# Performance work log

Measured on AMD Instinct MI355X. Metric: run time of the kernel, lower is better.

Reference implementation:

```python
import jax, jax.numpy as jnp
import numpy as np

DT = 0.1  # fixed RK4 step size from the constructor

def setup_inputs() -> dict:
    key = jax.random.key(0)
    k1, k2, k3 = jax.random.split(key, 3)
    B, U, H = 65536, 128, 512
    x0 = jax.random.normal(k1, (B, U), dtype=jnp.float32)
    # small init so 20 unrolled RK4 steps stay numerically tame
    W1 = jax.random.normal(k2, (U, H), dtype=jnp.float32) * (0.5 / np.sqrt(U))
    b1 = jnp.zeros((H,), dtype=jnp.float32)
    W2 = jax.random.normal(k3, (H, U), dtype=jnp.float32) * (0.5 / np.sqrt(H))
    b2 = jnp.zeros((U,), dtype=jnp.float32)
    return {"x0": x0, "W1": W1, "b1": b1, "W2": W2, "b2": b2}

def _mlp(x, W1, b1, W2, b2):
    # vector field: Dense(512, relu) -> Dense(128); time-independent
    return jnp.maximum(x @ W1 + b1, 0.0) @ W2 + b2

def _rk4_integrate(x, n_steps, W1, b1, W2, b2):
    def step(x, _):
        k1 = _mlp(x, W1, b1, W2, b2)
        k2 = _mlp(x + 0.5 * DT * k1, W1, b1, W2, b2)
        k3 = _mlp(x + 0.5 * DT * k2, W1, b1, W2, b2)
        k4 = _mlp(x + DT * k3, W1, b1, W2, b2)
        return x + (DT / 6.0) * (k1 + 2.0 * k2 + 2.0 * k3 + k4), None
    x, _ = jax.lax.scan(step, x, None, length=n_steps)
    return x

def reference(x0, W1, b1, W2, b2):
    # phase 1: integrate t in [0, t1/2 = 1.0] -> 10 RK4 steps at dt=0.1
    x = _rk4_integrate(x0, 10, W1, b1, W2, b2)
    # phase 2: n=5 macro-steps of length (1.0 - 0.0)/5 = 0.2 -> 2 RK4 steps each
    def macro(x, _):
        x = _rk4_integrate(x, 2, W1, b1, W2, b2)
        return x, None
    x, _ = jax.lax.scan(macro, x, None, length=5)
    return x
```

## Files before the change

kernel.cpp:

```cpp
#include <hip/hip_runtime.h>
#include <stdint.h>


typedef _Float16 half8 __attribute__((ext_vector_type(8)));
typedef float f32x4 __attribute__((ext_vector_type(4)));
typedef __attribute__((address_space(3))) char lchar;
typedef __attribute__((address_space(1))) char gchar;

#define KSTR 136

static __device__ __forceinline__ void gload_lds16(const void* g, void* l) {
  __builtin_amdgcn_global_load_lds((const gchar*)g, (lchar*)l, 16, 0, 0);
}

static __device__ __forceinline__ unsigned short f2h(float x) {
  union { _Float16 h; unsigned short u; } cv;
  cv.h = (_Float16)x;
  return cv.u;
}
static __device__ __forceinline__ float h2f(unsigned short u) {
  union { unsigned short u; _Float16 h; } cv;
  cv.u = u;
  return (float)cv.h;
}

__global__ void pack_w(const float* __restrict__ W1, const float* __restrict__ W2,
                       unsigned short* __restrict__ wp) {
  int id = blockIdx.x * 256 + threadIdx.x;
  int lane = id & 63, fid = (id >> 6) & 255;
  int g = lane >> 4, lm = lane & 15;
  int c = fid >> 4, f = fid & 15;
  if (f < 8) {
    int nt = f >> 2, ks = f & 3;
    int n = c * 32 + nt * 16 + lm;
#pragma unroll
    for (int j = 0; j < 8; ++j) {
      int k = ks * 32 + g * 8 + j;
      wp[fid * 512 + lane * 8 + j] = f2h(W1[k * 512 + n]);
    }
  } else {
    int nt = f - 8;
    int u = nt * 16 + lm;
#pragma unroll
    for (int j = 0; j < 8; ++j) {
      int k = c * 32 + g * 8 + j;
      wp[fid * 512 + lane * 8 + j] = f2h(W2[k * 128 + u]);
    }
  }
}

__global__ __launch_bounds__(512, 2) void node_rk4(
    const float* __restrict__ x0, const float* __restrict__ b1,
    const float* __restrict__ b2, const unsigned short* __restrict__ wp,
    float* __restrict__ out) {
  __shared__ char Wbuf[4][16384];
  __shared__ unsigned short stg[8][32][KSTR];
  __shared__ float b1s[512];
  __shared__ float b2s[128];

  const int tid = threadIdx.x;
  const int w = tid >> 6, lane = tid & 63;
  const int g = lane >> 4, lm = lane & 15;
  unsigned short(*stage)[KSTR] = stg[w];

  b1s[tid] = b1[tid];
  if (tid < 128) b2s[tid] = b2[tid];

  const int rbase = blockIdx.x * 256 + w * 32;
  f32x4 xa[2][8];
  ushort4 xbh[2][8];
#pragma unroll
  for (int mt = 0; mt < 2; ++mt)
#pragma unroll
    for (int t = 0; t < 8; ++t) {
      f32x4 v;
#pragma unroll
      for (int j = 0; j < 4; ++j)
        v[j] = x0[(rbase + mt * 16 + g * 4 + j) * 128 + t * 16 + lm];
      xa[mt][t] = v;
      ushort4 hq;
      hq.x = f2h(v[0]); hq.y = f2h(v[1]); hq.z = f2h(v[2]); hq.w = f2h(v[3]);
      xbh[mt][t] = hq;
#pragma unroll
      for (int j = 0; j < 4; ++j)
        stage[mt * 16 + g * 4 + j][t * 16 + lm] = (&hq.x)[j];
    }

#pragma unroll
  for (int pc = 0; pc < 3; ++pc) {
    const char* src = (const char*)wp + pc * 16384;
#pragma unroll
    for (int q = 0; q < 2; ++q) {
      int seg = w * 2 + q;
      gload_lds16(src + seg * 1024 + lane * 16, Wbuf[pc] + seg * 1024);
    }
  }
  asm volatile("s_waitcnt vmcnt(4) lgkmcnt(0)" ::: "memory");
  __builtin_amdgcn_s_barrier();

#pragma unroll 1
  for (int it = 0; it < 80; ++it) {
    const int s = it & 3;
    const float wgt = (s == 0 || s == 3) ? (0.1f / 6.0f) : (0.1f / 3.0f);
    const float alph = (s < 2) ? 0.05f : 0.1f;

    half8 A1[2][4];
#pragma unroll
    for (int mt = 0; mt < 2; ++mt)
#pragma unroll
      for (int ks = 0; ks < 4; ++ks)
        A1[mt][ks] = *(const half8*)&stage[mt * 16 + lm][ks * 32 + g * 8];

    f32x4 yacc[2][8];
#pragma unroll
    for (int mt = 0; mt < 2; ++mt)
#pragma unroll
      for (int t = 0; t < 8; ++t) yacc[mt][t] = f32x4{0.f, 0.f, 0.f, 0.f};

#pragma unroll
    for (int c = 0; c < 16; ++c) {
      {
        const int cn = (c + 3) & 15;
        char* buf = Wbuf[(c + 3) & 3];
        const char* src = (const char*)wp + cn * 16384;
#pragma unroll
        for (int q = 0; q < 2; ++q) {
          int seg = w * 2 + q;
          gload_lds16(src + seg * 1024 + lane * 16, buf + seg * 1024);
        }
      }
      const char* Wb = Wbuf[c & 3];

      __builtin_amdgcn_s_setprio(1);
#pragma unroll
      for (int nt = 0; nt < 2; ++nt) {
        f32x4 h0 = {0.f, 0.f, 0.f, 0.f}, h1 = {0.f, 0.f, 0.f, 0.f};
#pragma unroll
        for (int ks = 0; ks < 4; ++ks) {
          half8 bf = *(const half8*)(Wb + (nt * 4 + ks) * 1024 + lane * 16);
          h0 = __builtin_amdgcn_mfma_f32_16x16x32_f16(A1[0][ks], bf, h0, 0, 0, 0);
          h1 = __builtin_amdgcn_mfma_f32_16x16x32_f16(A1[1][ks], bf, h1, 0, 0, 0);
        }
        __builtin_amdgcn_s_setprio(0);
        float bb = b1s[c * 32 + nt * 16 + lm];
#pragma unroll
        for (int j = 0; j < 4; ++j) {
          stage[g * 4 + j][nt * 16 + lm] = f2h(fmaxf(h0[j] + bb, 0.f));
          stage[16 + g * 4 + j][nt * 16 + lm] = f2h(fmaxf(h1[j] + bb, 0.f));
        }
        __builtin_amdgcn_s_setprio(1);
      }

      half8 A2[2];
#pragma unroll
      for (int mt = 0; mt < 2; ++mt)
        A2[mt] = *(const half8*)&stage[mt * 16 + lm][g * 8];
#pragma unroll
      for (int nt = 0; nt < 8; ++nt) {
        half8 bf = *(const half8*)(Wb + 8192 + nt * 1024 + lane * 16);
        yacc[0][nt] = __builtin_amdgcn_mfma_f32_16x16x32_f16(A2[0], bf, yacc[0][nt], 0, 0, 0);
        yacc[1][nt] = __builtin_amdgcn_mfma_f32_16x16x32_f16(A2[1], bf, yacc[1][nt], 0, 0, 0);
      }
      __builtin_amdgcn_s_setprio(0);

      asm volatile("s_waitcnt vmcnt(4)" ::: "memory");
      __builtin_amdgcn_s_barrier();
    }

#pragma unroll
    for (int mt = 0; mt < 2; ++mt)
#pragma unroll
      for (int t = 0; t < 8; ++t) {
        f32x4 k = yacc[mt][t];
        float bb = b2s[t * 16 + lm];
#pragma unroll
        for (int j = 0; j < 4; ++j) k[j] += bb;
        xa[mt][t] += wgt * k;
        ushort4 hq;
        if (s == 3) {
          f32x4 v = xa[mt][t];
          hq.x = f2h(v[0]); hq.y = f2h(v[1]); hq.z = f2h(v[2]); hq.w = f2h(v[3]);
          xbh[mt][t] = hq;
        } else {
          ushort4 xq = xbh[mt][t];
          hq.x = f2h(h2f(xq.x) + alph * k[0]);
          hq.y = f2h(h2f(xq.y) + alph * k[1]);
          hq.z = f2h(h2f(xq.z) + alph * k[2]);
          hq.w = f2h(h2f(xq.w) + alph * k[3]);
        }
#pragma unroll
        for (int j = 0; j < 4; ++j)
          stage[mt * 16 + g * 4 + j][t * 16 + lm] = (&hq.x)[j];
      }
  }

#pragma unroll
  for (int mt = 0; mt < 2; ++mt)
#pragma unroll
    for (int t = 0; t < 8; ++t)
#pragma unroll
      for (int j = 0; j < 4; ++j)
        out[(rbase + mt * 16 + g * 4 + j) * 128 + t * 16 + lm] = xa[mt][t][j];
}

extern "C" void kernel_launch(void* const* d_in, const int* in_sizes, int n_in,
                              void* d_out, int out_size, void* d_ws, size_t ws_size,
                              hipStream_t stream) {
  const float* x0 = (const float*)d_in[0];
  const float* W1 = (const float*)d_in[1];
  const float* b1 = (const float*)d_in[2];
  const float* W2 = (const float*)d_in[3];
  const float* b2 = (const float*)d_in[4];
  float* out = (float*)d_out;

  unsigned short* wp = (unsigned short*)d_ws;

  pack_w<<<64, 256, 0, stream>>>(W1, W2, wp);
  node_rk4<<<256, 512, 0, stream>>>(x0, b1, b2, wp, out);
}
```

Before: 2.168 ms.

## Swap MFMA operand roles so accumulators pack into vectorized LDS stores

Both GEMMs now compute the transposed product: the weight fragment is the A operand and the activations are B. Each lane's four accumulator values then land at consecutive feature columns of one batch row, so they can be packed into a single 64-bit LDS store instead of four scattered 16-bit stores. The hidden activations move to a separate narrow staging buffer, and the global x0 loads and output stores become 16-byte vector accesses. This targets LDS store instruction count and bank traffic in the per-chunk ReLU write-back and the RK4 stage update. The cost is a little more LDS for the new buffer and 64-bit stores whose bank-conflict behaviour depends on the new strides.

```diff
diff --git a/kernel.cpp b/kernel.cpp
--- a/kernel.cpp
+++ b/kernel.cpp
@@ -7,7 +7,8 @@
 typedef __attribute__((address_space(3))) char lchar;
 typedef __attribute__((address_space(1))) char gchar;
 
-#define KSTR 136
+#define XSTR 136
+#define HSTR 40
 
 static __device__ __forceinline__ void gload_lds16(const void* g, void* l) {
   __builtin_amdgcn_global_load_lds((const gchar*)g, (lchar*)l, 16, 0, 0);
@@ -22,6 +23,12 @@
   union { unsigned short u; _Float16 h; } cv;
   cv.u = u;
   return (float)cv.h;
+}
+static __device__ __forceinline__ uint64_t pack4(float a, float b, float c, float d) {
+  union { _Float16 h[4]; uint64_t q; } cv;
+  cv.h[0] = (_Float16)a; cv.h[1] = (_Float16)b;
+  cv.h[2] = (_Float16)c; cv.h[3] = (_Float16)d;
+  return cv.q;
 }
 
 __global__ void pack_w(const float* __restrict__ W1, const float* __restrict__ W2,
@@ -31,20 +38,20 @@
   int g = lane >> 4, lm = lane & 15;
   int c = fid >> 4, f = fid & 15;
   if (f < 8) {
-    int nt = f >> 2, ks = f & 3;
-    int n = c * 32 + nt * 16 + lm;
+    int T = f >> 2, ks = f & 3;
+    int hid = c * 32 + T * 16 + lm;
 #pragma unroll
     for (int j = 0; j < 8; ++j) {
-      int k = ks * 32 + g * 8 + j;
-      wp[fid * 512 + lane * 8 + j] = f2h(W1[k * 512 + n]);
+      int kin = ks * 32 + g * 8 + j;
+      wp[fid * 512 + lane * 8 + j] = f2h(W1[kin * 512 + hid]);
     }
   } else {
-    int nt = f - 8;
-    int u = nt * 16 + lm;
+    int O = f - 8;
+    int of = O * 16 + lm;
 #pragma unroll
     for (int j = 0; j < 8; ++j) {
-      int k = c * 32 + g * 8 + j;
-      wp[fid * 512 + lane * 8 + j] = f2h(W2[k * 128 + u]);
+      int kh = c * 32 + g * 8 + j;
+      wp[fid * 512 + lane * 8 + j] = f2h(W2[kh * 128 + of]);
     }
   }
 }
@@ -54,14 +61,14 @@
     const float* __restrict__ b2, const unsigned short* __restrict__ wp,
     float* __restrict__ out) {
   __shared__ char Wbuf[4][16384];
-  __shared__ unsigned short stg[8][32][KSTR];
+  __shared__ __align__(16) unsigned short xs[8][32][XSTR];
+  __shared__ __align__(16) unsigned short hst[8][32][HSTR];
   __shared__ float b1s[512];
   __shared__ float b2s[128];
 
   const int tid = threadIdx.x;
   const int w = tid >> 6, lane = tid & 63;
   const int g = lane >> 4, lm = lane & 15;
-  unsigned short(*stage)[KSTR] = stg[w];
 
   b1s[tid] = b1[tid];
   if (tid < 128) b2s[tid] = b2[tid];
@@ -70,20 +77,16 @@
   f32x4 xa[2][8];
   ushort4 xbh[2][8];
 #pragma unroll
-  for (int mt = 0; mt < 2; ++mt)
-#pragma unroll
-    for (int t = 0; t < 8; ++t) {
-      f32x4 v;
-#pragma unroll
-      for (int j = 0; j < 4; ++j)
-        v[j] = x0[(rbase + mt * 16 + g * 4 + j) * 128 + t * 16 + lm];
-      xa[mt][t] = v;
+  for (int nt = 0; nt < 2; ++nt)
+#pragma unroll
+    for (int O = 0; O < 8; ++O) {
+      f32x4 v = *(const f32x4*)&x0[(rbase + nt * 16 + lm) * 128 + O * 16 + 4 * g];
+      xa[nt][O] = v;
+      uint64_t q = pack4(v[0], v[1], v[2], v[3]);
       ushort4 hq;
-      hq.x = f2h(v[0]); hq.y = f2h(v[1]); hq.z = f2h(v[2]); hq.w = f2h(v[3]);
-      xbh[mt][t] = hq;
-#pragma unroll
-      for (int j = 0; j < 4; ++j)
-        stage[mt * 16 + g * 4 + j][t * 16 + lm] = (&hq.x)[j];
+      *(uint64_t*)&hq = q;
+      xbh[nt][O] = hq;
+      *(uint64_t*)&xs[w][nt * 16 + lm][O * 16 + 4 * g] = q;
     }
 
 #pragma unroll
@@ -104,18 +107,18 @@
     const float wgt = (s == 0 || s == 3) ? (0.1f / 6.0f) : (0.1f / 3.0f);
     const float alph = (s < 2) ? 0.05f : 0.1f;
 
-    half8 A1[2][4];
-#pragma unroll
-    for (int mt = 0; mt < 2; ++mt)
+    half8 X1[2][4];
+#pragma unroll
+    for (int nt = 0; nt < 2; ++nt)
 #pragma unroll
       for (int ks = 0; ks < 4; ++ks)
-        A1[mt][ks] = *(const half8*)&stage[mt * 16 + lm][ks * 32 + g * 8];
+        X1[nt][ks] = *(const half8*)&xs[w][nt * 16 + lm][ks * 32 + g * 8];
 
     f32x4 yacc[2][8];
 #pragma unroll
-    for (int mt = 0; mt < 2; ++mt)
-#pragma unroll
-      for (int t = 0; t < 8; ++t) yacc[mt][t] = f32x4{0.f, 0.f, 0.f, 0.f};
+    for (int nt = 0; nt < 2; ++nt)
+#pragma unroll
+      for (int O = 0; O < 8; ++O) yacc[nt][O] = f32x4{0.f, 0.f, 0.f, 0.f};
 
 #pragma unroll
     for (int c = 0; c < 16; ++c) {
@@ -133,33 +136,32 @@
 
       __builtin_amdgcn_s_setprio(1);
 #pragma unroll
-      for (int nt = 0; nt < 2; ++nt) {
+      for (int T = 0; T < 2; ++T) {
         f32x4 h0 = {0.f, 0.f, 0.f, 0.f}, h1 = {0.f, 0.f, 0.f, 0.f};
 #pragma unroll
         for (int ks = 0; ks < 4; ++ks) {
-          half8 bf = *(const half8*)(Wb + (nt * 4 + ks) * 1024 + lane * 16);
-          h0 = __builtin_amdgcn_mfma_f32_16x16x32_f16(A1[0][ks], bf, h0, 0, 0, 0);
-          h1 = __builtin_amdgcn_mfma_f32_16x16x32_f16(A1[1][ks], bf, h1, 0, 0, 0);
+          half8 wa = *(const half8*)(Wb + (T * 4 + ks) * 1024 + lane * 16);
+          h0 = __builtin_amdgcn_mfma_f32_16x16x32_f16(wa, X1[0][ks], h0, 0, 0, 0);
+          h1 = __builtin_amdgcn_mfma_f32_16x16x32_f16(wa, X1[1][ks], h1, 0, 0, 0);
         }
         __builtin_amdgcn_s_setprio(0);
-        float bb = b1s[c * 32 + nt * 16 + lm];
-#pragma unroll
-        for (int j = 0; j < 4; ++j) {
-          stage[g * 4 + j][nt * 16 + lm] = f2h(fmaxf(h0[j] + bb, 0.f));
-          stage[16 + g * 4 + j][nt * 16 + lm] = f2h(fmaxf(h1[j] + bb, 0.f));
-        }
+        f32x4 bb = *(const f32x4*)&b1s[c * 32 + T * 16 + 4 * g];
+        uint64_t p0 = pack4(fmaxf(h0[0] + bb[0], 0.f), fmaxf(h0[1] + bb[1], 0.f),
+                            fmaxf(h0[2] + bb[2], 0.f), fmaxf(h0[3] + bb[3], 0.f));
+        uint64_t p1 = pack4(fmaxf(h1[0] + bb[0], 0.f), fmaxf(h1[1] + bb[1], 0.f),
+                            fmaxf(h1[2] + bb[2], 0.f), fmaxf(h1[3] + bb[3], 0.f));
+        *(uint64_t*)&hst[w][lm][T * 16 + 4 * g] = p0;
+        *(uint64_t*)&hst[w][16 + lm][T * 16 + 4 * g] = p1;
         __builtin_amdgcn_s_setprio(1);
       }
 
-      half8 A2[2];
-#pragma unroll
-      for (int mt = 0; mt < 2; ++mt)
-        A2[mt] = *(const half8*)&stage[mt * 16 + lm][g * 8];
-#pragma unroll
-      for (int nt = 0; nt < 8; ++nt) {
-        half8 bf = *(const half8*)(Wb + 8192 + nt * 1024 + lane * 16);
-        yacc[0][nt] = __builtin_amdgcn_mfma_f32_16x16x32_f16(A2[0], bf, yacc[0][nt], 0, 0, 0);
-        yacc[1][nt] = __builtin_amdgcn_mfma_f32_16x16x32_f16(A2[1], bf, yacc[1][nt], 0, 0, 0);
+      half8 H20 = *(const half8*)&hst[w][lm][g * 8];
+      half8 H21 = *(const half8*)&hst[w][16 + lm][g * 8];
+#pragma unroll
+      for (int O = 0; O < 8; ++O) {
+        half8 wa = *(const half8*)(Wb + 8192 + O * 1024 + lane * 16);
+        yacc[0][O] = __builtin_amdgcn_mfma_f32_16x16x32_f16(wa, H20, yacc[0][O], 0, 0, 0);
+        yacc[1][O] = __builtin_amdgcn_mfma_f32_16x16x32_f16(wa, H21, yacc[1][O], 0, 0, 0);
       }
       __builtin_amdgcn_s_setprio(0);
 
@@ -168,39 +170,35 @@
     }
 
 #pragma unroll
-    for (int mt = 0; mt < 2; ++mt)
-#pragma unroll
-      for (int t = 0; t < 8; ++t) {
-        f32x4 k = yacc[mt][t];
-        float bb = b2s[t * 16 + lm];
-#pragma unroll
-        for (int j = 0; j < 4; ++j) k[j] += bb;
-        xa[mt][t] += wgt * k;
-        ushort4 hq;
+    for (int nt = 0; nt < 2; ++nt)
+#pragma unroll
+      for (int O = 0; O < 8; ++O) {
+        f32x4 bb2 = *(const f32x4*)&b2s[O * 16 + 4 * g];
+        f32x4 k = yacc[nt][O];
+#pragma unroll
+        for (int j = 0; j < 4; ++j) k[j] += bb2[j];
+        xa[nt][O] += wgt * k;
+        uint64_t q;
         if (s == 3) {
-          f32x4 v = xa[mt][t];
-          hq.x = f2h(v[0]); hq.y = f2h(v[1]); hq.z = f2h(v[2]); hq.w = f2h(v[3]);
-          xbh[mt][t] = hq;
+          f32x4 v = xa[nt][O];
+          q = pack4(v[0], v[1], v[2], v[3]);
+          ushort4 hq;
+          *(uint64_t*)&hq = q;
+          xbh[nt][O] = hq;
         } else {
-          ushort4 xq = xbh[mt][t];
-          hq.x = f2h(h2f(xq.x) + alph * k[0]);
-          hq.y = f2h(h2f(xq.y) + alph * k[1]);
-          hq.z = f2h(h2f(xq.z) + alph * k[2]);
-          hq.w = f2h(h2f(xq.w) + alph * k[3]);
+          ushort4 xq = xbh[nt][O];
+          q = pack4(h2f(xq.x) + alph * k[0], h2f(xq.y) + alph * k[1],
+                    h2f(xq.z) + alph * k[2], h2f(xq.w) + alph * k[3]);
         }
-#pragma unroll
-        for (int j = 0; j < 4; ++j)
-          stage[mt * 16 + g * 4 + j][t * 16 + lm] = (&hq.x)[j];
+        *(uint64_t*)&xs[w][nt * 16 + lm][O * 16 + 4 * g] = q;
       }
   }
 
 #pragma unroll
-  for (int mt = 0; mt < 2; ++mt)
-#pragma unroll
-    for (int t = 0; t < 8; ++t)
-#pragma unroll
-      for (int j = 0; j < 4; ++j)
-        out[(rbase + mt * 16 + g * 4 + j) * 128 + t * 16 + lm] = xa[mt][t][j];
+  for (int nt = 0; nt < 2; ++nt)
+#pragma unroll
+    for (int O = 0; O < 8; ++O)
+      *(f32x4*)&out[(rbase + nt * 16 + lm) * 128 + O * 16 + 4 * g] = xa[nt][O];
 }
 
 extern "C" void kernel_launch(void* const* d_in, const int* in_sizes, int n_in,
```

Result: faster. 2.091 ms (-3.5%).
